# Performance work log

Measured on AMD Instinct MI355X. Metric: run time of the kernel, lower is better.

## Reference

```python
import jax, jax.numpy as jnp
import numpy as np
import math

D_MODEL = 1024
NUM_HEADS = 16
MAX_LEN = 2048
D_HEAD = D_MODEL // NUM_HEADS
BATCH = 2
SEQ = 2048


def setup_inputs() -> dict:
    root = jax.random.key(0)
    ks = jax.random.split(root, 10)
    s = 1.0 / math.sqrt(D_MODEL)
    return {
        "query": jax.random.normal(ks[0], (BATCH, SEQ, D_MODEL), jnp.float32),
        "key": jax.random.normal(ks[1], (BATCH, SEQ, D_MODEL), jnp.float32),
        "value": jax.random.normal(ks[2], (BATCH, SEQ, D_MODEL), jnp.float32),
        "Wq": jax.random.normal(ks[3], (D_MODEL, D_MODEL), jnp.float32) * s,
        "bq": jax.random.normal(ks[4], (D_MODEL,), jnp.float32) * s,
        "Wk": jax.random.normal(ks[5], (D_MODEL, D_MODEL), jnp.float32) * s,
        "bk": jax.random.normal(ks[6], (D_MODEL,), jnp.float32) * s,
        "Wv": jax.random.normal(ks[7], (D_MODEL, D_MODEL), jnp.float32) * s,
        "bv": jax.random.normal(ks[8], (D_MODEL,), jnp.float32) * s,
        "Er": jax.random.normal(ks[9], (MAX_LEN, D_HEAD), jnp.float32),
    }


def _skew(QEr):
    # QEr: [B, H, S, S] -> pad one zero column on the left, reshape, drop first row
    B, H, R, C = QEr.shape
    padded = jnp.pad(QEr, ((0, 0), (0, 0), (0, 0), (1, 0)))  # [B,H,R,C+1]
    reshaped = padded.reshape(B, H, C + 1, R)
    return reshaped[:, :, 1:, :]  # [B,H,R,C] == Srel


def reference(query, key, value, Wq, bq, Wk, bk, Wv, bv, Er):
    B, S, D = query.shape
    H, dh = NUM_HEADS, D_HEAD
    # nn.Linear: x @ W.T + b
    q = (jnp.einsum("bsd,ed->bse", query, Wq) + bq).reshape(B, S, H, dh).transpose(0, 2, 1, 3)  # [B,H,S,dh]
    k = (jnp.einsum("bsd,ed->bse", key, Wk) + bk).reshape(B, S, H, dh).transpose(0, 2, 1, 3)
    v = (jnp.einsum("bsd,ed->bse", value, Wv) + bv).reshape(B, S, H, dh).transpose(0, 2, 1, 3)
    start = MAX_LEN - S
    Er_s = Er[start:, :]  # [S, dh]
    QEr = jnp.einsum("bhsd,ld->bhsl", q, Er_s)  # [B,H,S,S]
    Srel = _skew(QEr)
    QK = jnp.einsum("bhsd,bhtd->bhst", q, k)
    attn = (QK + Srel) / math.sqrt(dh)
    causal = jnp.tril(jnp.ones((S, S), dtype=bool))
    attn = jnp.where(causal[None, None], attn, -jnp.inf)
    attn = jax.nn.softmax(attn, axis=-1)
    out = jnp.einsum("bhst,bhtd->bhsd", attn, v)  # [B,H,S,dh]
    out = out.transpose(0, 2, 1, 3).reshape(B, S, D)
    return out  # dropout is identity in eval mode
```

## Files before the change

kernel.cpp:

```cpp
#include <hip/hip_runtime.h>
#include <hip/hip_bf16.h>

typedef __attribute__((ext_vector_type(8))) short bf16x8;
typedef __attribute__((ext_vector_type(4))) float f32x4;

#define DEVI __device__ __forceinline__

constexpr int SEQ_   = 2048;
constexpr int HEADS  = 16;
constexpr int DHEAD  = 64;
constexpr int DMODEL = 1024;

DEVI unsigned short f2bf(float x) {
  __hip_bfloat16 h = __float2bfloat16(x);
  return __builtin_bit_cast(unsigned short, h);
}

DEVI f32x4 MFMA(bf16x8 a, bf16x8 b, f32x4 c) {
  return __builtin_amdgcn_mfma_f32_16x16x32_bf16(a, b, c, 0, 0, 0);
}

__global__ void conv3_kernel(const float* s0, const float* s1, const float* s2,
                             unsigned short* d0, unsigned short* d1, unsigned short* d2,
                             int n) {
  const float* s = (blockIdx.y == 0) ? s0 : (blockIdx.y == 1) ? s1 : s2;
  unsigned short* d = (blockIdx.y == 0) ? d0 : (blockIdx.y == 1) ? d1 : d2;
  int i = (blockIdx.x * 256 + threadIdx.x) * 8;
  if (i >= n) return;
  const float4* p = (const float4*)(s + i);
  float4 v0 = p[0], v1 = p[1];
  union { unsigned short u[8]; bf16x8 v; } t;
  t.u[0] = f2bf(v0.x); t.u[1] = f2bf(v0.y); t.u[2] = f2bf(v0.z); t.u[3] = f2bf(v0.w);
  t.u[4] = f2bf(v1.x); t.u[5] = f2bf(v1.y); t.u[6] = f2bf(v1.z); t.u[7] = f2bf(v1.w);
  *(bf16x8*)(d + i) = t.v;
}

__global__ __launch_bounds__(256) void proj3_kernel(
    const unsigned short* __restrict__ X0, const unsigned short* __restrict__ X1,
    const unsigned short* __restrict__ X2,
    const unsigned short* __restrict__ W0, const unsigned short* __restrict__ W1,
    const unsigned short* __restrict__ W2,
    const float* __restrict__ bi0, const float* __restrict__ bi1,
    const float* __restrict__ bi2,
    unsigned short* __restrict__ o0, unsigned short* __restrict__ o1,
    unsigned short* __restrict__ o2) {
  const int z = blockIdx.z;
  const unsigned short* X = (z == 0) ? X0 : (z == 1) ? X1 : X2;
  const unsigned short* W = (z == 0) ? W0 : (z == 1) ? W1 : W2;
  const float* bias        = (z == 0) ? bi0 : (z == 1) ? bi1 : bi2;
  unsigned short* out      = (z == 0) ? o0 : (z == 1) ? o1 : o2;

  __shared__ unsigned short Abuf[2][128 * 32];
  __shared__ unsigned short Bbuf[2][128 * 32];
  const int tid  = threadIdx.x;
  const int lane = tid & 63, wv = tid >> 6;
  const int q = lane >> 4, r = lane & 15;
  const int wrow = wv >> 1, wcol = wv & 1;
  const int rowA0 = blockIdx.x * 128, colB0 = blockIdx.y * 128;

  const char* Ag = (const char*)(X + (size_t)rowA0 * DMODEL);
  const char* Bg = (const char*)(W + (size_t)colB0 * DMODEL);

  f32x4 acc[4][4] = {};

  auto stage = [&](int ks, int buf) {
    const int koff = ks * 64;
#pragma unroll
    for (int i = 0; i < 2; ++i) {
      const int b   = (i * 256 + tid) * 16;
      const int row = b >> 6, col = b & 63;
      __builtin_amdgcn_global_load_lds(
          (const __attribute__((address_space(1))) void*)(Ag + (size_t)row * (DMODEL * 2) + koff + col),
          (__attribute__((address_space(3))) void*)((char*)&Abuf[buf][0] + i * 4096 + wv * 1024),
          16, 0, 0);
      __builtin_amdgcn_global_load_lds(
          (const __attribute__((address_space(1))) void*)(Bg + (size_t)row * (DMODEL * 2) + koff + col),
          (__attribute__((address_space(3))) void*)((char*)&Bbuf[buf][0] + i * 4096 + wv * 1024),
          16, 0, 0);
    }
  };

  stage(0, 0);
  for (int ks = 0; ks < 32; ++ks) {
    __syncthreads();
    if (ks + 1 < 32) stage(ks + 1, (ks + 1) & 1);
    const unsigned short* A  = &Abuf[ks & 1][0];
    const unsigned short* Bt = &Bbuf[ks & 1][0];
    bf16x8 af[4], bfr[4];
#pragma unroll
    for (int t = 0; t < 4; ++t) {
      af[t]  = *(const bf16x8*)(A  + (wrow * 64 + t * 16 + r) * 32 + q * 8);
      bfr[t] = *(const bf16x8*)(Bt + (wcol * 64 + t * 16 + r) * 32 + q * 8);
    }
#pragma unroll
    for (int m = 0; m < 4; ++m)
#pragma unroll
      for (int n = 0; n < 4; ++n)
        acc[m][n] = MFMA(af[m], bfr[n], acc[m][n]);
  }

#pragma unroll
  for (int m = 0; m < 4; ++m) {
#pragma unroll
    for (int n = 0; n < 4; ++n) {
      const int e  = colB0 + wcol * 64 + n * 16 + r;
      const float bv = bias[e];
      const int h = e >> 6, dd = e & 63;
      const int nrow0 = rowA0 + wrow * 64 + m * 16 + q * 4;
      const int bb = nrow0 >> 11, ss0 = nrow0 & 2047;
      const size_t bh = (size_t)(bb * HEADS + h);
      if (z == 0) {
#pragma unroll
        for (int j = 0; j < 4; ++j)
          out[(bh * SEQ_ + (ss0 + j)) * DHEAD + dd] = f2bf(acc[m][n][j] + bv);
      } else if (z == 1) {
        const int kc = dd >> 5, d32 = dd & 31;
#pragma unroll
        for (int j = 0; j < 4; ++j) {
          const int s = ss0 + j;
          out[(((bh * 64 + (s >> 5)) * 2 + kc) * 32 + (s & 31)) * 32 + d32] =
              f2bf(acc[m][n][j] + bv);
        }
      } else {
        const int stile = ss0 >> 5, st = ss0 & 31;
        union { unsigned short u[4]; uint2 v; } pk;
#pragma unroll
        for (int j = 0; j < 4; ++j) pk.u[j] = f2bf(acc[m][n][j] + bv);
        *(uint2*)&out[((bh * 64 + stile) * 64 + dd) * 32 + st] = pk.v;
      }
    }
  }
}

__global__ __launch_bounds__(128, 2) void attn_kernel(const unsigned short* __restrict__ qb,
                                                      const unsigned short* __restrict__ kt,
                                                      const unsigned short* __restrict__ vt,
                                                      const unsigned short* __restrict__ Er,
                                                      float* __restrict__ out) {
  __shared__ unsigned short k_lds[2][2048];
  __shared__ unsigned short v_lds[2][2048];
  __shared__ unsigned short p_lds[2][16][40];

  const int tid  = threadIdx.x;
  const int lane = tid & 63, wv = tid >> 6;
  const int q = lane >> 4, r = lane & 15;

  const int lid = blockIdx.x;
  const int xcd = lid & 7, idx = lid >> 3;
  const int bh  = (xcd << 2) | (idx & 3);
  const int pairidx = idx >> 2;
  const int bb = bh >> 4, hh = bh & 15;

  const unsigned short* qbh = qb + (size_t)bh * SEQ_ * DHEAD;
  const char* ktb = (const char*)(kt + (size_t)bh * 64 * 2048);
  const char* vtb = (const char*)(vt + (size_t)bh * 64 * 2048);

  const f32x4 zero4 = {0.f, 0.f, 0.f, 0.f};

  auto stage = [&](int tile, int buf) {
#pragma unroll
    for (int c = 0; c < 2; ++c) {
      __builtin_amdgcn_global_load_lds(
          (const __attribute__((address_space(1))) void*)(ktb + (size_t)tile * 4096 + (c * 128 + tid) * 16),
          (__attribute__((address_space(3))) void*)((char*)&k_lds[buf][0] + c * 2048 + wv * 1024),
          16, 0, 0);
      __builtin_amdgcn_global_load_lds(
          (const __attribute__((address_space(1))) void*)(vtb + (size_t)tile * 4096 + (c * 128 + tid) * 16),
          (__attribute__((address_space(3))) void*)((char*)&v_lds[buf][0] + c * 2048 + wv * 1024),
          16, 0, 0);
    }
  };

#pragma unroll 1
  for (int si = 0; si < 2; ++si) {
    const int t = si ? pairidx : 63 - pairidx;
    const int nIter = t + 1;
    const int s0 = t * 32 + wv * 16;

    __syncthreads();
    stage(0, 0);

    bf16x8 qf0 = *(const bf16x8*)(qbh + (size_t)(s0 + r) * DHEAD + q * 8);
    bf16x8 qf1 = *(const bf16x8*)(qbh + (size_t)(s0 + r) * DHEAD + 32 + q * 8);

    f32x4 oacc[4] = {};
    float lpart[4] = {0.f, 0.f, 0.f, 0.f};
    f32x4 qer0;
    {
      const int l0 = 2032 - s0 + r;
      bf16x8 e00 = *(const bf16x8*)(Er + (size_t)l0 * DHEAD + q * 8);
      bf16x8 e01 = *(const bf16x8*)(Er + (size_t)l0 * DHEAD + 32 + q * 8);
      qer0 = MFMA(qf1, e01, MFMA(qf0, e00, zero4));
    }

#pragma unroll 1
    for (int it = 0; it < nIter; ++it) {
      const int cur = it & 1;
      const int t0 = it * 32;
      const int lbase = 2032 + t0 - s0;

      __syncthreads();

      int l1 = lbase + 16 + r; l1 = l1 < 2047 ? l1 : 2047;
      int l2 = lbase + 32 + r; l2 = l2 < 2047 ? l2 : 2047;
      bf16x8 e10 = *(const bf16x8*)(Er + (size_t)l1 * DHEAD + q * 8);
      bf16x8 e11 = *(const bf16x8*)(Er + (size_t)l1 * DHEAD + 32 + q * 8);
      bf16x8 e20 = *(const bf16x8*)(Er + (size_t)l2 * DHEAD + q * 8);
      bf16x8 e21 = *(const bf16x8*)(Er + (size_t)l2 * DHEAD + 32 + q * 8);

      if (it + 1 < nIter) stage(it + 1, 1 - cur);

      const unsigned short* KL = &k_lds[cur][0];
      const unsigned short* VL = &v_lds[cur][0];
      bf16x8 kf00 = *(const bf16x8*)(KL + r * 32 + q * 8);
      bf16x8 kf01 = *(const bf16x8*)(KL + 1024 + r * 32 + q * 8);
      bf16x8 kf10 = *(const bf16x8*)(KL + (16 + r) * 32 + q * 8);
      bf16x8 kf11 = *(const bf16x8*)(KL + 1024 + (16 + r) * 32 + q * 8);

      __builtin_amdgcn_s_setprio(1);
      f32x4 s40  = MFMA(qf1, kf01, MFMA(qf0, kf00, zero4));
      f32x4 s41  = MFMA(qf1, kf11, MFMA(qf0, kf10, zero4));
      f32x4 qer1 = MFMA(qf1, e11, MFMA(qf0, e10, zero4));
      f32x4 qer2 = MFMA(qf1, e21, MFMA(qf0, e20, zero4));
      __builtin_amdgcn_s_setprio(0);

#pragma unroll
      for (int j = 0; j < 4; ++j) {
        const int sl = q * 4 + j;
        const int idxw = r + 15 - sl;
        const int srcl = (q << 4) | (idxw & 15);
        const float g0 = __shfl(qer0[j], srcl);
        const float g1 = __shfl(qer1[j], srcl);
        const float g2 = __shfl(qer2[j], srcl);
        const bool lo = (idxw < 16);
        float sv0 = (s40[j] + (lo ? g0 : g1)) * 0.125f;
        float sv1 = (s41[j] + (lo ? g1 : g2)) * 0.125f;
        if (t0 + r      > s0 + sl) sv0 = -1e30f;
        if (t0 + 16 + r > s0 + sl) sv1 = -1e30f;
        const float p0 = __expf(sv0);
        const float p1 = __expf(sv1);
        lpart[j] += p0 + p1;
        p_lds[wv][sl][r]      = f2bf(p0);
        p_lds[wv][sl][16 + r] = f2bf(p1);
      }

      bf16x8 pf = *(const bf16x8*)(&p_lds[wv][r][0] + q * 8);
      bf16x8 vf0 = *(const bf16x8*)(VL + (r) * 32 + q * 8);
      bf16x8 vf1 = *(const bf16x8*)(VL + (16 + r) * 32 + q * 8);
      bf16x8 vf2 = *(const bf16x8*)(VL + (32 + r) * 32 + q * 8);
      bf16x8 vf3 = *(const bf16x8*)(VL + (48 + r) * 32 + q * 8);
      __builtin_amdgcn_s_setprio(1);
      oacc[0] = MFMA(pf, vf0, oacc[0]);
      oacc[1] = MFMA(pf, vf1, oacc[1]);
      oacc[2] = MFMA(pf, vf2, oacc[2]);
      oacc[3] = MFMA(pf, vf3, oacc[3]);
      __builtin_amdgcn_s_setprio(0);
      qer0 = qer2;
    }

#pragma unroll
    for (int j = 0; j < 4; ++j) {
      float ls = lpart[j];
#pragma unroll
      for (int d = 1; d < 16; d <<= 1) ls += __shfl_xor(ls, d);
      const float inv = 1.0f / ls;
      const int ss = s0 + q * 4 + j;
#pragma unroll
      for (int dc = 0; dc < 4; ++dc) {
        const int dd = dc * 16 + r;
        out[((size_t)(bb * SEQ_ + ss)) * DMODEL + hh * DHEAD + dd] = oacc[dc][j] * inv;
      }
    }
  }
}

extern "C" void kernel_launch(void* const* d_in, const int* in_sizes, int n_in,
                              void* d_out, int out_size, void* d_ws, size_t ws_size,
                              hipStream_t stream) {
  const float* query = (const float*)d_in[0];
  const float* key   = (const float*)d_in[1];
  const float* value = (const float*)d_in[2];
  const float* Wq    = (const float*)d_in[3];
  const float* bq    = (const float*)d_in[4];
  const float* Wk    = (const float*)d_in[5];
  const float* bk    = (const float*)d_in[6];
  const float* Wv    = (const float*)d_in[7];
  const float* bv    = (const float*)d_in[8];
  const float* Er    = (const float*)d_in[9];

  char* ws = (char*)d_ws;
  unsigned short* qb   = (unsigned short*)(ws + (0u  << 20));
  unsigned short* ktil = (unsigned short*)(ws + (8u  << 20));
  unsigned short* vtil = (unsigned short*)(ws + (16u << 20));
  unsigned short* Xq   = (unsigned short*)(ws + (32u << 20));
  unsigned short* Xk   = (unsigned short*)(ws + (40u << 20));
  unsigned short* Xv   = (unsigned short*)(ws + (48u << 20));
  unsigned short* Wqb  = (unsigned short*)(ws + (56u << 20));
  unsigned short* Wkb  = (unsigned short*)(ws + (58u << 20));
  unsigned short* Wvb  = (unsigned short*)(ws + (60u << 20));
  unsigned short* Erb  = (unsigned short*)(ws + (62u << 20));

  conv3_kernel<<<dim3(2048, 3), 256, 0, stream>>>(query, key, value, Xq, Xk, Xv,
                                                  2 * SEQ_ * DMODEL);
  conv3_kernel<<<dim3(512, 3), 256, 0, stream>>>(Wq, Wk, Wv, Wqb, Wkb, Wvb,
                                                 DMODEL * DMODEL);
  conv3_kernel<<<dim3(64, 1), 256, 0, stream>>>(Er, Er, Er, Erb, Erb, Erb,
                                                SEQ_ * DHEAD);

  proj3_kernel<<<dim3(32, 8, 3), 256, 0, stream>>>(Xq, Xk, Xv, Wqb, Wkb, Wvb,
                                                   bq, bk, bv, qb, ktil, vtil);

  attn_kernel<<<dim3(1024), 128, 0, stream>>>(qb, ktil, vtil, Erb, (float*)d_out);
}
```

Before: 146.0 us.

## Restructure attention into 8-wave blocks sharing K/V tiles, fold scale into Q

The attention kernel now launches 512 blocks of 8 waves. Each block covers 128 query rows of one head and shares each staged K/V tile across all eight waves, instead of 2-wave blocks that processed two paired query tiles in sequence. The loop is manually double-buffered with Er fragments prefetched one step ahead, and waves whose rows are fully masked skip compute. The K/V tile layouts are reordered so LDS fragment reads become contiguous per lane. The 1/sqrt(dh) scale is folded into the Q projection, and the W and Er conversions are merged into one launch. Load balance now relies on the T ordering, and larger blocks may reduce occupancy.

```diff
diff --git a/kernel.cpp b/kernel.cpp
--- a/kernel.cpp
+++ b/kernel.cpp
@@ -25,6 +25,25 @@
                              int n) {
   const float* s = (blockIdx.y == 0) ? s0 : (blockIdx.y == 1) ? s1 : s2;
   unsigned short* d = (blockIdx.y == 0) ? d0 : (blockIdx.y == 1) ? d1 : d2;
+  int i = (blockIdx.x * 256 + threadIdx.x) * 8;
+  if (i >= n) return;
+  const float4* p = (const float4*)(s + i);
+  float4 v0 = p[0], v1 = p[1];
+  union { unsigned short u[8]; bf16x8 v; } t;
+  t.u[0] = f2bf(v0.x); t.u[1] = f2bf(v0.y); t.u[2] = f2bf(v0.z); t.u[3] = f2bf(v0.w);
+  t.u[4] = f2bf(v1.x); t.u[5] = f2bf(v1.y); t.u[6] = f2bf(v1.z); t.u[7] = f2bf(v1.w);
+  *(bf16x8*)(d + i) = t.v;
+}
+
+__global__ void conv4_kernel(const float* s0, const float* s1, const float* s2,
+                             const float* s3,
+                             unsigned short* d0, unsigned short* d1,
+                             unsigned short* d2, unsigned short* d3,
+                             int n_w, int n_e) {
+  const int y = blockIdx.y;
+  const float* s = (y == 0) ? s0 : (y == 1) ? s1 : (y == 2) ? s2 : s3;
+  unsigned short* d = (y == 0) ? d0 : (y == 1) ? d1 : (y == 2) ? d2 : d3;
+  const int n = (y == 3) ? n_e : n_w;
   int i = (blockIdx.x * 256 + threadIdx.x) * 8;
   if (i >= n) return;
   const float4* p = (const float4*)(s + i);
@@ -112,34 +131,40 @@
       if (z == 0) {
 #pragma unroll
         for (int j = 0; j < 4; ++j)
-          out[(bh * SEQ_ + (ss0 + j)) * DHEAD + dd] = f2bf(acc[m][n][j] + bv);
+          out[(bh * SEQ_ + (ss0 + j)) * DHEAD + dd] = f2bf((acc[m][n][j] + bv) * 0.125f);
       } else if (z == 1) {
-        const int kc = dd >> 5, d32 = dd & 31;
 #pragma unroll
         for (int j = 0; j < 4; ++j) {
           const int s = ss0 + j;
-          out[(((bh * 64 + (s >> 5)) * 2 + kc) * 32 + (s & 31)) * 32 + d32] =
-              f2bf(acc[m][n][j] + bv);
+          const size_t off = (bh * 64 + (size_t)(s >> 5)) * 2048
+                           + (size_t)(((dd >> 5) * 2 + ((s >> 4) & 1)) * 512)
+                           + (size_t)(((((dd & 31) >> 3) << 4) + (s & 15)) * 8)
+                           + (dd & 7);
+          out[off] = f2bf(acc[m][n][j] + bv);
         }
       } else {
-        const int stile = ss0 >> 5, st = ss0 & 31;
         union { unsigned short u[4]; uint2 v; } pk;
 #pragma unroll
         for (int j = 0; j < 4; ++j) pk.u[j] = f2bf(acc[m][n][j] + bv);
-        *(uint2*)&out[((bh * 64 + stile) * 64 + dd) * 32 + st] = pk.v;
+        const size_t off = (bh * 64 + (size_t)(ss0 >> 5)) * 2048
+                         + (size_t)((dd >> 4) * 512)
+                         + (size_t)(((((ss0 & 31) >> 3) << 4) + (dd & 15)) * 8)
+                         + (ss0 & 7);
+        *(uint2*)&out[off] = pk.v;
       }
     }
   }
 }
 
-__global__ __launch_bounds__(128, 2) void attn_kernel(const unsigned short* __restrict__ qb,
-                                                      const unsigned short* __restrict__ kt,
-                                                      const unsigned short* __restrict__ vt,
-                                                      const unsigned short* __restrict__ Er,
-                                                      float* __restrict__ out) {
+struct ErF { bf16x8 e10, e11, e20, e21; };
+
+__global__ __launch_bounds__(512, 4) void attn_kernel(
+    const unsigned short* __restrict__ qb, const unsigned short* __restrict__ kt,
+    const unsigned short* __restrict__ vt, const unsigned short* __restrict__ Er,
+    float* __restrict__ out) {
   __shared__ unsigned short k_lds[2][2048];
   __shared__ unsigned short v_lds[2][2048];
-  __shared__ unsigned short p_lds[2][16][40];
+  __shared__ unsigned short p_lds[8][16][40];
 
   const int tid  = threadIdx.x;
   const int lane = tid & 63, wv = tid >> 6;
@@ -148,128 +173,127 @@
   const int lid = blockIdx.x;
   const int xcd = lid & 7, idx = lid >> 3;
   const int bh  = (xcd << 2) | (idx & 3);
-  const int pairidx = idx >> 2;
+  const int T   = 15 - (idx >> 2);
+  const int s0  = T * 128 + wv * 16;
+  const int nIter = 4 * T + 4;
   const int bb = bh >> 4, hh = bh & 15;
 
   const unsigned short* qbh = qb + (size_t)bh * SEQ_ * DHEAD;
   const char* ktb = (const char*)(kt + (size_t)bh * 64 * 2048);
   const char* vtb = (const char*)(vt + (size_t)bh * 64 * 2048);
-
   const f32x4 zero4 = {0.f, 0.f, 0.f, 0.f};
 
+  const bool isK = (tid < 256);
+  const char* sbase = isK ? ktb : vtb;
+  const int subt = tid & 255;
+
   auto stage = [&](int tile, int buf) {
-#pragma unroll
-    for (int c = 0; c < 2; ++c) {
-      __builtin_amdgcn_global_load_lds(
-          (const __attribute__((address_space(1))) void*)(ktb + (size_t)tile * 4096 + (c * 128 + tid) * 16),
-          (__attribute__((address_space(3))) void*)((char*)&k_lds[buf][0] + c * 2048 + wv * 1024),
-          16, 0, 0);
-      __builtin_amdgcn_global_load_lds(
-          (const __attribute__((address_space(1))) void*)(vtb + (size_t)tile * 4096 + (c * 128 + tid) * 16),
-          (__attribute__((address_space(3))) void*)((char*)&v_lds[buf][0] + c * 2048 + wv * 1024),
-          16, 0, 0);
-    }
+    char* dst = (char*)(isK ? &k_lds[buf][0] : &v_lds[buf][0]) + (wv & 3) * 1024;
+    __builtin_amdgcn_global_load_lds(
+        (const __attribute__((address_space(1))) void*)(sbase + (size_t)tile * 4096 + subt * 16),
+        (__attribute__((address_space(3))) void*)dst, 16, 0, 0);
   };
 
-#pragma unroll 1
-  for (int si = 0; si < 2; ++si) {
-    const int t = si ? pairidx : 63 - pairidx;
-    const int nIter = t + 1;
-    const int s0 = t * 32 + wv * 16;
-
+  auto loadE = [&](ErF& e, int it2) {
+    const int lb = 2032 + it2 * 32 - s0;
+    int l1 = lb + 16 + r; l1 = l1 < 2047 ? l1 : 2047;
+    int l2 = lb + 32 + r; l2 = l2 < 2047 ? l2 : 2047;
+    e.e10 = *(const bf16x8*)(Er + (size_t)l1 * DHEAD + q * 8);
+    e.e11 = *(const bf16x8*)(Er + (size_t)l1 * DHEAD + 32 + q * 8);
+    e.e20 = *(const bf16x8*)(Er + (size_t)l2 * DHEAD + q * 8);
+    e.e21 = *(const bf16x8*)(Er + (size_t)l2 * DHEAD + 32 + q * 8);
+  };
+
+  stage(0, 0);
+  bf16x8 qf0 = *(const bf16x8*)(qbh + (size_t)(s0 + r) * DHEAD + q * 8);
+  bf16x8 qf1 = *(const bf16x8*)(qbh + (size_t)(s0 + r) * DHEAD + 32 + q * 8);
+
+  f32x4 oacc[4] = {};
+  float lpart[4] = {0.f, 0.f, 0.f, 0.f};
+  f32x4 qer0;
+  {
+    const int l0 = 2032 - s0 + r;
+    bf16x8 e00 = *(const bf16x8*)(Er + (size_t)l0 * DHEAD + q * 8);
+    bf16x8 e01 = *(const bf16x8*)(Er + (size_t)l0 * DHEAD + 32 + q * 8);
+    qer0 = MFMA(qf1, e01, MFMA(qf0, e00, zero4));
+  }
+
+  auto body = [&](int it, int cur, const ErF& e) {
+    const int t0 = it * 32;
+    if (t0 > s0 + 15) return;
+    const unsigned short* KL = &k_lds[cur][0];
+    const unsigned short* VL = &v_lds[cur][0];
+    bf16x8 kf00 = *(const bf16x8*)(KL + lane * 8);
+    bf16x8 kf10 = *(const bf16x8*)(KL + 512 + lane * 8);
+    bf16x8 kf01 = *(const bf16x8*)(KL + 1024 + lane * 8);
+    bf16x8 kf11 = *(const bf16x8*)(KL + 1536 + lane * 8);
+
+    __builtin_amdgcn_s_setprio(1);
+    f32x4 s40  = MFMA(qf1, kf01, MFMA(qf0, kf00, zero4));
+    f32x4 s41  = MFMA(qf1, kf11, MFMA(qf0, kf10, zero4));
+    f32x4 qer1 = MFMA(qf1, e.e11, MFMA(qf0, e.e10, zero4));
+    f32x4 qer2 = MFMA(qf1, e.e21, MFMA(qf0, e.e20, zero4));
+    __builtin_amdgcn_s_setprio(0);
+
+    const int d0 = t0 - s0;
+#pragma unroll
+    for (int j = 0; j < 4; ++j) {
+      const int sl = q * 4 + j;
+      const int idxw = r + 15 - sl;
+      const int srcl = (q << 4) | (idxw & 15);
+      const float g0s = __shfl(qer0[j], srcl);
+      const float g1s = __shfl(qer1[j], srcl);
+      const float g2s = __shfl(qer2[j], srcl);
+      const bool lo = (idxw < 16);
+      const float sv0 = s40[j] + (lo ? g0s : g1s);
+      const float sv1 = s41[j] + (lo ? g1s : g2s);
+      const int a = sl - r;
+      const float p0 = (a >= d0)      ? __expf(sv0) : 0.f;
+      const float p1 = (a >= d0 + 16) ? __expf(sv1) : 0.f;
+      lpart[j] += p0 + p1;
+      p_lds[wv][sl][r]      = f2bf(p0);
+      p_lds[wv][sl][16 + r] = f2bf(p1);
+    }
+
+    bf16x8 pf  = *(const bf16x8*)(&p_lds[wv][r][0] + q * 8);
+    bf16x8 vf0 = *(const bf16x8*)(VL + lane * 8);
+    bf16x8 vf1 = *(const bf16x8*)(VL + 512 + lane * 8);
+    bf16x8 vf2 = *(const bf16x8*)(VL + 1024 + lane * 8);
+    bf16x8 vf3 = *(const bf16x8*)(VL + 1536 + lane * 8);
+    __builtin_amdgcn_s_setprio(1);
+    oacc[0] = MFMA(pf, vf0, oacc[0]);
+    oacc[1] = MFMA(pf, vf1, oacc[1]);
+    oacc[2] = MFMA(pf, vf2, oacc[2]);
+    oacc[3] = MFMA(pf, vf3, oacc[3]);
+    __builtin_amdgcn_s_setprio(0);
+    qer0 = qer2;
+  };
+
+  ErF eA, eB;
+  loadE(eA, 0);
+  int it = 0;
+  while (true) {
     __syncthreads();
-    stage(0, 0);
-
-    bf16x8 qf0 = *(const bf16x8*)(qbh + (size_t)(s0 + r) * DHEAD + q * 8);
-    bf16x8 qf1 = *(const bf16x8*)(qbh + (size_t)(s0 + r) * DHEAD + 32 + q * 8);
-
-    f32x4 oacc[4] = {};
-    float lpart[4] = {0.f, 0.f, 0.f, 0.f};
-    f32x4 qer0;
-    {
-      const int l0 = 2032 - s0 + r;
-      bf16x8 e00 = *(const bf16x8*)(Er + (size_t)l0 * DHEAD + q * 8);
-      bf16x8 e01 = *(const bf16x8*)(Er + (size_t)l0 * DHEAD + 32 + q * 8);
-      qer0 = MFMA(qf1, e01, MFMA(qf0, e00, zero4));
-    }
-
-#pragma unroll 1
-    for (int it = 0; it < nIter; ++it) {
-      const int cur = it & 1;
-      const int t0 = it * 32;
-      const int lbase = 2032 + t0 - s0;
-
-      __syncthreads();
-
-      int l1 = lbase + 16 + r; l1 = l1 < 2047 ? l1 : 2047;
-      int l2 = lbase + 32 + r; l2 = l2 < 2047 ? l2 : 2047;
-      bf16x8 e10 = *(const bf16x8*)(Er + (size_t)l1 * DHEAD + q * 8);
-      bf16x8 e11 = *(const bf16x8*)(Er + (size_t)l1 * DHEAD + 32 + q * 8);
-      bf16x8 e20 = *(const bf16x8*)(Er + (size_t)l2 * DHEAD + q * 8);
-      bf16x8 e21 = *(const bf16x8*)(Er + (size_t)l2 * DHEAD + 32 + q * 8);
-
-      if (it + 1 < nIter) stage(it + 1, 1 - cur);
-
-      const unsigned short* KL = &k_lds[cur][0];
-      const unsigned short* VL = &v_lds[cur][0];
-      bf16x8 kf00 = *(const bf16x8*)(KL + r * 32 + q * 8);
-      bf16x8 kf01 = *(const bf16x8*)(KL + 1024 + r * 32 + q * 8);
-      bf16x8 kf10 = *(const bf16x8*)(KL + (16 + r) * 32 + q * 8);
-      bf16x8 kf11 = *(const bf16x8*)(KL + 1024 + (16 + r) * 32 + q * 8);
-
-      __builtin_amdgcn_s_setprio(1);
-      f32x4 s40  = MFMA(qf1, kf01, MFMA(qf0, kf00, zero4));
-      f32x4 s41  = MFMA(qf1, kf11, MFMA(qf0, kf10, zero4));
-      f32x4 qer1 = MFMA(qf1, e11, MFMA(qf0, e10, zero4));
-      f32x4 qer2 = MFMA(qf1, e21, MFMA(qf0, e20, zero4));
-      __builtin_amdgcn_s_setprio(0);
-
-#pragma unroll
-      for (int j = 0; j < 4; ++j) {
-        const int sl = q * 4 + j;
-        const int idxw = r + 15 - sl;
-        const int srcl = (q << 4) | (idxw & 15);
-        const float g0 = __shfl(qer0[j], srcl);
-        const float g1 = __shfl(qer1[j], srcl);
-        const float g2 = __shfl(qer2[j], srcl);
-        const bool lo = (idxw < 16);
-        float sv0 = (s40[j] + (lo ? g0 : g1)) * 0.125f;
-        float sv1 = (s41[j] + (lo ? g1 : g2)) * 0.125f;
-        if (t0 + r      > s0 + sl) sv0 = -1e30f;
-        if (t0 + 16 + r > s0 + sl) sv1 = -1e30f;
-        const float p0 = __expf(sv0);
-        const float p1 = __expf(sv1);
-        lpart[j] += p0 + p1;
-        p_lds[wv][sl][r]      = f2bf(p0);
-        p_lds[wv][sl][16 + r] = f2bf(p1);
-      }
-
-      bf16x8 pf = *(const bf16x8*)(&p_lds[wv][r][0] + q * 8);
-      bf16x8 vf0 = *(const bf16x8*)(VL + (r) * 32 + q * 8);
-      bf16x8 vf1 = *(const bf16x8*)(VL + (16 + r) * 32 + q * 8);
-      bf16x8 vf2 = *(const bf16x8*)(VL + (32 + r) * 32 + q * 8);
-      bf16x8 vf3 = *(const bf16x8*)(VL + (48 + r) * 32 + q * 8);
-      __builtin_amdgcn_s_setprio(1);
-      oacc[0] = MFMA(pf, vf0, oacc[0]);
-      oacc[1] = MFMA(pf, vf1, oacc[1]);
-      oacc[2] = MFMA(pf, vf2, oacc[2]);
-      oacc[3] = MFMA(pf, vf3, oacc[3]);
-      __builtin_amdgcn_s_setprio(0);
-      qer0 = qer2;
-    }
-
-#pragma unroll
-    for (int j = 0; j < 4; ++j) {
-      float ls = lpart[j];
-#pragma unroll
-      for (int d = 1; d < 16; d <<= 1) ls += __shfl_xor(ls, d);
-      const float inv = 1.0f / ls;
-      const int ss = s0 + q * 4 + j;
-#pragma unroll
-      for (int dc = 0; dc < 4; ++dc) {
-        const int dd = dc * 16 + r;
-        out[((size_t)(bb * SEQ_ + ss)) * DMODEL + hh * DHEAD + dd] = oacc[dc][j] * inv;
-      }
+    if (it + 1 < nIter) { stage(it + 1, 1); loadE(eB, it + 1); }
+    body(it, 0, eA);
+    if (++it >= nIter) break;
+    __syncthreads();
+    if (it + 1 < nIter) { stage(it + 1, 0); loadE(eA, it + 1); }
+    body(it, 1, eB);
+    if (++it >= nIter) break;
+  }
+
+#pragma unroll
+  for (int j = 0; j < 4; ++j) {
+    float ls = lpart[j];
+#pragma unroll
+    for (int d = 1; d < 16; d <<= 1) ls += __shfl_xor(ls, d);
+    const float inv = 1.0f / ls;
+    const int ss = s0 + q * 4 + j;
+#pragma unroll
+    for (int dc = 0; dc < 4; ++dc) {
+      const int dd = dc * 16 + r;
+      out[((size_t)(bb * SEQ_ + ss)) * DMODEL + hh * DHEAD + dd] = oacc[dc][j] * inv;
     }
   }
 }
@@ -302,13 +326,12 @@
 
   conv3_kernel<<<dim3(2048, 3), 256, 0, stream>>>(query, key, value, Xq, Xk, Xv,
                                                   2 * SEQ_ * DMODEL);
-  conv3_kernel<<<dim3(512, 3), 256, 0, stream>>>(Wq, Wk, Wv, Wqb, Wkb, Wvb,
-                                                 DMODEL * DMODEL);
-  conv3_kernel<<<dim3(64, 1), 256, 0, stream>>>(Er, Er, Er, Erb, Erb, Erb,
-                                                SEQ_ * DHEAD);
+  conv4_kernel<<<dim3(512, 4), 256, 0, stream>>>(Wq, Wk, Wv, Er,
+                                                 Wqb, Wkb, Wvb, Erb,
+                                                 DMODEL * DMODEL, SEQ_ * DHEAD);
 
   proj3_kernel<<<dim3(32, 8, 3), 256, 0, stream>>>(Xq, Xk, Xv, Wqb, Wkb, Wvb,
                                                    bq, bk, bv, qb, ktil, vtil);
 
-  attn_kernel<<<dim3(1024), 128, 0, stream>>>(qb, ktil, vtil, Erb, (float*)d_out);
-}
+  attn_kernel<<<dim3(512), 512, 0, stream>>>(qb, ktil, vtil, Erb, (float*)d_out);
+}
```

Result: slower. 163.8 us (+12.2%).
